# Optimization experiments

Measured on AMD Instinct MI355X. Metric: run time of the kernel, lower is better.

The kernel has to match this reference:

```python
import jax, jax.numpy as jnp
import numpy as np

FEATS = 768
HEAD = 12
HD = FEATS // HEAD


def setup_inputs() -> dict:
    key = jax.random.key(0)
    ks = jax.random.split(key, 10)
    b, n, f = 8, 1024, FEATS
    s = 1.0 / np.sqrt(f)
    return {
        "x": jax.random.normal(ks[0], (b, n, f), dtype=jnp.float32),
        "bias": jnp.zeros((), dtype=jnp.float32),
        "Wq": jax.random.normal(ks[1], (f, f), dtype=jnp.float32) * s,
        "bq": jnp.zeros((f,), dtype=jnp.float32),
        "Wk": jax.random.normal(ks[2], (f, f), dtype=jnp.float32) * s,
        "bk": jnp.zeros((f,), dtype=jnp.float32),
        "Wv": jax.random.normal(ks[3], (f, f), dtype=jnp.float32) * s,
        "bv": jnp.zeros((f,), dtype=jnp.float32),
        "Wo": jax.random.normal(ks[4], (f, f), dtype=jnp.float32) * s,
        "bo": jnp.zeros((f,), dtype=jnp.float32),
    }


def reference(x, bias, Wq, bq, Wk, bk, Wv, bv, Wo, bo):
    b, n, f = x.shape
    sqrt_d = jnp.sqrt(jnp.asarray(f, dtype=x.dtype))  # scale uses full feats, per source

    def split_heads(t):  # (b,n,f) -> (b,h,n,hd)
        return t.reshape(b, n, HEAD, HD).transpose(0, 2, 1, 3)

    q = split_heads(x @ Wq.T + bq)
    k = split_heads(x @ Wk.T + bk)
    v = split_heads(x @ Wv.T + bv)

    # sigmoid attention: no row-wise normalization
    score = jax.nn.sigmoid(jnp.einsum('bhif,bhjf->bhij', q, k) / sqrt_d + bias)
    attn = jnp.einsum('bhij,bhjf->bihf', score, v)  # (b,n,h,hd)
    o = attn.reshape(b, n, f) @ Wo.T + bo  # dropout p=0.0 -> identity
    return o
```

## Files before the change

### kernel.cpp

```cpp
#include <hip/hip_runtime.h>

#define FEATS 768
#define NHEAD 12
#define HD    64
#define SEQ   1024
#define NB    8
#define MROWS (NB*SEQ)
#define NQK   (2*FEATS)
#define QKVN  (3*FEATS)
#define QSC   0.0520616136f

typedef __attribute__((ext_vector_type(8))) __bf16          bf16x8;
typedef __attribute__((ext_vector_type(4))) __bf16          bf16x4;
typedef __attribute__((ext_vector_type(4))) unsigned short  us4;
typedef __attribute__((ext_vector_type(4))) float           f32x4;

__device__ __forceinline__ unsigned short f2bf(float f) {
  union { float f; unsigned u; } v; v.f = f;
  return (unsigned short)((v.u + 0x7fffu + ((v.u >> 16) & 1u)) >> 16);
}

__device__ __forceinline__ void gload_lds16(const void* g, void* l) {
  __builtin_amdgcn_global_load_lds(
      (const __attribute__((address_space(1))) void*)g,
      (__attribute__((address_space(3))) void*)l, 16, 0, 0);
}

__global__ void cast_all(const float* __restrict__ x,
                         const float* __restrict__ Wq, const float* __restrict__ Wk,
                         const float* __restrict__ Wv, const float* __restrict__ Wo,
                         const float* __restrict__ bq, const float* __restrict__ bk,
                         const float* __restrict__ bv,
                         unsigned short* __restrict__ Xbf,
                         unsigned short* __restrict__ Wcat,
                         unsigned short* __restrict__ Wobf,
                         float* __restrict__ bcat) {
  int blk = blockIdx.x;
  if (blk < 6144) {
    int i = blk * 256 + threadIdx.x;
    f32x4 v = ((const f32x4*)x)[i];
    us4 o;
    o[0] = f2bf(v[0]); o[1] = f2bf(v[1]); o[2] = f2bf(v[2]); o[3] = f2bf(v[3]);
    ((us4*)Xbf)[i] = o;
  } else if (blk < 8448) {
    int bb = blk - 6144;
    int mtx = bb / 576;
    int i = (bb % 576) * 256 + threadIdx.x;
    const float* src = (mtx == 0) ? Wq : (mtx == 1) ? Wk : (mtx == 2) ? Wv : Wo;
    f32x4 v = ((const f32x4*)src)[i];
    us4 o;
    o[0] = f2bf(v[0]); o[1] = f2bf(v[1]); o[2] = f2bf(v[2]); o[3] = f2bf(v[3]);
    if (mtx < 3) ((us4*)Wcat)[mtx * 147456 + i] = o;
    else         ((us4*)Wobf)[i] = o;
  } else {
    int i = (blk - 8448) * 256 + threadIdx.x;
    if (i < QKVN)
      bcat[i] = (i < FEATS) ? bq[i] : (i < 2*FEATS ? bk[i-FEATS] : bv[i-2*FEATS]);
  }
}

#define FOFF(row) ((row)*64 + (((g) ^ (((row) >> 1) & 3)) << 4))

__global__ __launch_bounds__(256, 3) void gemm1_bt(
    const unsigned short* __restrict__ A,
    const unsigned short* __restrict__ B,
    const float* __restrict__ bias,
    unsigned short* __restrict__ QKo,
    unsigned short* __restrict__ VTo)
{
  __shared__ __align__(16) char Al[2 * 8192];
  __shared__ __align__(16) char Bl[2 * 12288];

  const int tid  = threadIdx.x;
  const int lane = tid & 63;
  const int w    = tid >> 6;
  const int l15  = lane & 15;
  const int g    = lane >> 4;
  const int wm   = (w >> 1) * 64;
  const int wn   = (w & 1) * 96;

  const int id  = blockIdx.x;
  const int xcd = id & 7;
  const int j   = id >> 3;
  const int mi  = xcd * 8 + (j & 7);
  const int ni  = j >> 3;
  const int mbase = mi * 128;
  const int nbase = ni * 192;

  const int trow  = tid >> 2;
  const int sslot = ((tid & 3) ^ ((tid >> 3) & 3)) * 8;
  const unsigned short* Ag = A + (size_t)(mbase + trow) * 768 + sslot;
  const unsigned short* Bg = B + (size_t)(nbase + trow) * 768 + sslot;

  auto STAGE = [&](int buf, int t) {
    const unsigned short* sa = Ag + t * 32;
    const unsigned short* sb = Bg + t * 32;
    char* da = Al + buf * 8192  + tid * 16;
    char* db = Bl + buf * 12288 + tid * 16;
    gload_lds16(sa,            da);
    gload_lds16(sa + 64*768,   da + 4096);
    gload_lds16(sb,            db);
    gload_lds16(sb + 64*768,   db + 4096);
    gload_lds16(sb + 128*768,  db + 8192);
  };

  f32x4 acc[4][6] = {};

  STAGE(0, 0);
  asm volatile("s_waitcnt vmcnt(0)" ::: "memory");
  __builtin_amdgcn_s_barrier();

  for (int t = 0; t < 24; t++) {
    if (t < 23) STAGE((t + 1) & 1, t + 1);

    const char* Ab = Al + (t & 1) * 8192;
    const char* Bb = Bl + (t & 1) * 12288;
    bf16x8 af[4];
#pragma unroll
    for (int mf = 0; mf < 4; mf++) {
      const int row = wm + mf*16 + l15;
      af[mf] = *(const bf16x8*)(Ab + FOFF(row));
    }
    __builtin_amdgcn_s_setprio(1);
#pragma unroll
    for (int nf = 0; nf < 6; nf++) {
      const int row = wn + nf*16 + l15;
      bf16x8 bfv = *(const bf16x8*)(Bb + FOFF(row));
#pragma unroll
      for (int mf = 0; mf < 4; mf++)
        acc[mf][nf] = __builtin_amdgcn_mfma_f32_16x16x32_bf16(af[mf], bfv, acc[mf][nf], 0, 0, 0);
    }
    __builtin_amdgcn_s_setprio(0);

    if (t < 23) {
      asm volatile("s_waitcnt vmcnt(0)" ::: "memory");
      __builtin_amdgcn_s_barrier();
    }
  }

  const bool isQK = (ni < 8);
  const float osc = (ni < 4) ? QSC : 1.0f;
#pragma unroll
  for (int mf = 0; mf < 4; mf++)
#pragma unroll
    for (int nf = 0; nf < 6; nf++) {
      const int col  = nbase + wn + nf*16 + l15;
      const float bb = bias[col];
      const int row0 = mbase + wm + mf*16 + g*4;
      if (isQK) {
#pragma unroll
        for (int r = 0; r < 4; r++)
          QKo[(size_t)(row0 + r)*NQK + col] = f2bf((acc[mf][nf][r] + bb) * osc);
      } else {
        const int c  = col - NQK;
        const int hh = c >> 6, dd = c & 63;
        const int bI = row0 >> 10, n0 = row0 & 1023;
        us4 o;
#pragma unroll
        for (int r = 0; r < 4; r++) o[r] = f2bf(acc[mf][nf][r] + bb);
        *(us4*)(VTo + ((size_t)((bI*NHEAD + hh)*HD + dd))*SEQ + n0) = o;
      }
    }
}

__global__ __launch_bounds__(256, 4) void gemm2_bt(
    const unsigned short* __restrict__ A,
    const unsigned short* __restrict__ B,
    const float* __restrict__ bias,
    float* __restrict__ C)
{
  __shared__ __align__(16) char Al[2 * 4096];
  __shared__ __align__(16) char Bl[2 * 8192];

  const int tid  = threadIdx.x;
  const int lane = tid & 63;
  const int w    = tid >> 6;
  const int l15  = lane & 15;
  const int g    = lane >> 4;
  const int wm   = (w >> 1) * 32;
  const int wn   = (w & 1) * 64;

  const int id  = blockIdx.x;
  const int xcd = id & 7;
  const int j   = id >> 3;
  const int mi  = xcd * 16 + (j & 15);
  const int ni  = j >> 4;
  const int mbase = mi * 64;
  const int nbase = ni * 128;

  const int trow  = tid >> 2;
  const int sslot = ((tid & 3) ^ ((tid >> 3) & 3)) * 8;
  const unsigned short* Ag = A + (size_t)(mbase + trow) * 768 + sslot;
  const unsigned short* Bg = B + (size_t)(nbase + trow) * 768 + sslot;

  auto STAGE = [&](int buf, int t) {
    const unsigned short* sa = Ag + t * 32;
    const unsigned short* sb = Bg + t * 32;
    char* da = Al + buf * 4096 + tid * 16;
    char* db = Bl + buf * 8192 + tid * 16;
    gload_lds16(sa,           da);
    gload_lds16(sb,           db);
    gload_lds16(sb + 64*768,  db + 4096);
  };

  f32x4 acc[2][4] = {};

  STAGE(0, 0);
  asm volatile("s_waitcnt vmcnt(0)" ::: "memory");
  __builtin_amdgcn_s_barrier();

  for (int t = 0; t < 24; t++) {
    if (t < 23) STAGE((t + 1) & 1, t + 1);

    const char* Ab = Al + (t & 1) * 4096;
    const char* Bb = Bl + (t & 1) * 8192;
    bf16x8 af[2], bfv[4];
#pragma unroll
    for (int mf = 0; mf < 2; mf++) {
      const int row = wm + mf*16 + l15;
      af[mf] = *(const bf16x8*)(Ab + FOFF(row));
    }
#pragma unroll
    for (int nf = 0; nf < 4; nf++) {
      const int row = wn + nf*16 + l15;
      bfv[nf] = *(const bf16x8*)(Bb + FOFF(row));
    }
    __builtin_amdgcn_s_setprio(1);
#pragma unroll
    for (int mf = 0; mf < 2; mf++)
#pragma unroll
      for (int nf = 0; nf < 4; nf++)
        acc[mf][nf] = __builtin_amdgcn_mfma_f32_16x16x32_bf16(af[mf], bfv[nf], acc[mf][nf], 0, 0, 0);
    __builtin_amdgcn_s_setprio(0);

    if (t < 23) {
      asm volatile("s_waitcnt vmcnt(0)" ::: "memory");
      __builtin_amdgcn_s_barrier();
    }
  }

#pragma unroll
  for (int mf = 0; mf < 2; mf++)
#pragma unroll
    for (int nf = 0; nf < 4; nf++) {
      const int col  = nbase + wn + nf*16 + l15;
      const float bb = bias[col];
      const int row0 = mbase + wm + mf*16 + g*4;
#pragma unroll
      for (int r = 0; r < 4; r++)
        C[(size_t)(row0 + r)*FEATS + col] = acc[mf][nf][r] + bb;
    }
}
#undef FOFF

__global__ __launch_bounds__(256, 3) void attn_kernel(
    const unsigned short* __restrict__ QK,
    const unsigned short* __restrict__ VT,
    const float* __restrict__ biasp,
    unsigned short* __restrict__ AO)
{
  __shared__ __align__(16) char Kl[2][8192];
  __shared__ __align__(16) char Vl[2][8192];
  __shared__ __align__(16) char Sl[4][4096];

  const int tid  = threadIdx.x;
  const int lane = tid & 63;
  const int w    = tid >> 6;
  const int l15  = lane & 15;
  const int g    = lane >> 4;

  const int id  = blockIdx.x;
  const int r8  = id & 7;
  const int m   = id >> 3;
  const int bh  = r8 * 12 + (m >> 3);
  const int qx  = m & 7;
  const int b   = bh / NHEAD;
  const int h   = bh % NHEAD;
  const int rowB  = b * SEQ;
  const int qbase = rowB + qx * 128;

  const float Kb = __builtin_amdgcn_exp2f(-biasp[0] * 1.4426950408889634f);

  bf16x8 qf[2][2];
  {
    const unsigned short* qp = QK + (size_t)(qbase + w*32 + l15) * NQK + h*HD + g*8;
    qf[0][0] = *(const bf16x8*)(qp);
    qf[0][1] = *(const bf16x8*)(qp + 32);
    qf[1][0] = *(const bf16x8*)(qp + 16*NQK);
    qf[1][1] = *(const bf16x8*)(qp + 16*NQK + 32);
  }

  const int trow = tid >> 3;
  const int colb = ((tid & 7) * 16) ^ ((trow & 7) << 4);
  const char* Ksrc = (const char*)QK +
      ((size_t)(rowB + trow) * NQK + FEATS + h*HD) * 2 + colb;
  const char* Vsrc = (const char*)VT +
      ((size_t)(bh*HD + trow)) * (SEQ*2) + colb;

  auto STAGE = [&](int p, int t) {
    char* kw = Kl[p] + tid*16;
    char* vw = Vl[p] + tid*16;
    gload_lds16(Ksrc + (size_t)t * 64 * (NQK*2),                kw);
    gload_lds16(Ksrc + (size_t)t * 64 * (NQK*2) + 32*(NQK*2),   kw + 4096);
    gload_lds16(Vsrc + t * 128,                                 vw);
    gload_lds16(Vsrc + t * 128 + 32*(SEQ*2),                    vw + 4096);
  };

  char* Sw = Sl[w];
  f32x4 o_acc[4][2] = {};

  STAGE(0, 0);
  __syncthreads();

  for (int t = 0; t < 16; t++) {
    const int p = t & 1;
    if (t < 15) STAGE(p ^ 1, t + 1);

    const char* Kp = Kl[p];
    f32x4 sT[2][4] = {};
    __builtin_amdgcn_s_setprio(1);
#pragma unroll
    for (int nf = 0; nf < 4; nf++)
#pragma unroll
      for (int ks = 0; ks < 2; ks++) {
        const int row = nf*16 + l15;
        const int by  = (row*128 + ks*64 + g*16) ^ ((row & 7) << 4);
        bf16x8 kf = *(const bf16x8*)(Kp + by);
        sT[0][nf] = __builtin_amdgcn_mfma_f32_16x16x32_bf16(kf, qf[0][ks], sT[0][nf], 0, 0, 0);
        sT[1][nf] = __builtin_amdgcn_mfma_f32_16x16x32_bf16(kf, qf[1][ks], sT[1][nf], 0, 0, 0);
      }
    __builtin_amdgcn_s_setprio(0);

    const char* Vp = Vl[p];
    bf16x8 vf[4][2];
#pragma unroll
    for (int df = 0; df < 4; df++)
#pragma unroll
      for (int js = 0; js < 2; js++) {
        const int row = df*16 + l15;
        const int by  = (row*128 + js*64 + g*16) ^ ((row & 7) << 4);
        vf[df][js] = *(const bf16x8*)(Vp + by);
      }

#pragma unroll
    for (int qm = 0; qm < 2; qm++)
#pragma unroll
      for (int nf = 0; nf < 4; nf++) {
        bf16x4 pk;
#pragma unroll
        for (int rr = 0; rr < 4; rr++) {
          const float e = __builtin_amdgcn_exp2f(-sT[qm][nf][rr]);
          pk[rr] = (__bf16)__builtin_amdgcn_rcpf(__builtin_fmaf(Kb, e, 1.0f));
        }
        const int sq = qm*16 + l15;
        const int by = (sq*128 + (nf*16 + g*4)*2) ^ ((sq & 7) << 4);
        *(bf16x4*)(Sw + by) = pk;
      }

    __builtin_amdgcn_s_setprio(1);
#pragma unroll
    for (int js = 0; js < 2; js++) {
      bf16x8 sf[2];
#pragma unroll
      for (int qm = 0; qm < 2; qm++) {
        const int sq = qm*16 + l15;
        const int by = (sq*128 + js*64 + g*16) ^ ((sq & 7) << 4);
        sf[qm] = *(const bf16x8*)(Sw + by);
      }
#pragma unroll
      for (int df = 0; df < 4; df++)
#pragma unroll
        for (int qm = 0; qm < 2; qm++)
          o_acc[df][qm] = __builtin_amdgcn_mfma_f32_16x16x32_bf16(vf[df][js], sf[qm], o_acc[df][qm], 0, 0, 0);
    }
    __builtin_amdgcn_s_setprio(0);

    __syncthreads();
  }

  unsigned short* aop = AO + (size_t)(qbase + w*32) * FEATS + h*HD;
#pragma unroll
  for (int df = 0; df < 4; df++)
#pragma unroll
    for (int qm = 0; qm < 2; qm++) {
      const int q  = qm*16 + l15;
      const int d0 = df*16 + g*4;
      bf16x4 o;
#pragma unroll
      for (int rr = 0; rr < 4; rr++) o[rr] = (__bf16)o_acc[df][qm][rr];
      *(bf16x4*)(aop + (size_t)q * FEATS + d0) = o;
    }
}

extern "C" void kernel_launch(void* const* d_in, const int* in_sizes, int n_in,
                              void* d_out, int out_size, void* d_ws, size_t ws_size,
                              hipStream_t stream) {
  const float* x    = (const float*)d_in[0];
  const float* bias = (const float*)d_in[1];
  const float* Wq   = (const float*)d_in[2];
  const float* bq   = (const float*)d_in[3];
  const float* Wk   = (const float*)d_in[4];
  const float* bk   = (const float*)d_in[5];
  const float* Wv   = (const float*)d_in[6];
  const float* bv   = (const float*)d_in[7];
  const float* Wo   = (const float*)d_in[8];
  const float* bo   = (const float*)d_in[9];
  float* out = (float*)d_out;

  char* ws = (char*)d_ws;
  unsigned short* Xbf  = (unsigned short*)(ws + 0);
  unsigned short* Wcat = (unsigned short*)(ws + 12582912);
  unsigned short* Wobf = (unsigned short*)(ws + 16121856);
  float*          bcat = (float*)        (ws + 17301504);
  unsigned short* QKb  = (unsigned short*)(ws + 17310720);
  unsigned short* VTb  = (unsigned short*)(ws + 42476544);
  unsigned short* AO   = Xbf;

  cast_all<<<8457, 256, 0, stream>>>(x, Wq, Wk, Wv, Wo, bq, bk, bv,
                                     Xbf, Wcat, Wobf, bcat);

  gemm1_bt<<<768, 256, 0, stream>>>(Xbf, Wcat, bcat, QKb, VTb);

  attn_kernel<<<768, 256, 0, stream>>>(QKb, VTb, bias, AO);

  gemm2_bt<<<768, 256, 0, stream>>>(AO, Wobf, bo, out);
}
```

Baseline: 108.6 us.

## Software-pipeline attention loop: overlap QK^T of tile t with sigmoid·V of t-1

Restructures the sigmoid-attention inner loop so each iteration computes the QK^T MFMAs for tile t while applying sigmoid and the PV MFMAs for tile t-1. Score accumulators ping-pong between two register sets, and K and V staging are split so V is loaded one tile later than K. The goal is to hide exp/rcp and LDS latency behind MFMA work and to keep the matrix units busy. In exchange it needs more accumulator registers, which can lower occupancy, and the schedule is more complex.

```diff
diff --git a/kernel.cpp b/kernel.cpp
--- a/kernel.cpp
+++ b/kernel.cpp
@@ -297,51 +297,22 @@
   const char* Vsrc = (const char*)VT +
       ((size_t)(bh*HD + trow)) * (SEQ*2) + colb;
 
-  auto STAGE = [&](int p, int t) {
+  auto STAGE_K = [&](int p, int t) {
     char* kw = Kl[p] + tid*16;
+    gload_lds16(Ksrc + (size_t)t * 64 * (NQK*2),              kw);
+    gload_lds16(Ksrc + (size_t)t * 64 * (NQK*2) + 32*(NQK*2), kw + 4096);
+  };
+  auto STAGE_V = [&](int p, int t) {
     char* vw = Vl[p] + tid*16;
-    gload_lds16(Ksrc + (size_t)t * 64 * (NQK*2),                kw);
-    gload_lds16(Ksrc + (size_t)t * 64 * (NQK*2) + 32*(NQK*2),   kw + 4096);
-    gload_lds16(Vsrc + t * 128,                                 vw);
-    gload_lds16(Vsrc + t * 128 + 32*(SEQ*2),                    vw + 4096);
+    gload_lds16(Vsrc + t * 128,              vw);
+    gload_lds16(Vsrc + t * 128 + 32*(SEQ*2), vw + 4096);
   };
 
   char* Sw = Sl[w];
   f32x4 o_acc[4][2] = {};
-
-  STAGE(0, 0);
-  __syncthreads();
-
-  for (int t = 0; t < 16; t++) {
-    const int p = t & 1;
-    if (t < 15) STAGE(p ^ 1, t + 1);
-
-    const char* Kp = Kl[p];
-    f32x4 sT[2][4] = {};
-    __builtin_amdgcn_s_setprio(1);
-#pragma unroll
-    for (int nf = 0; nf < 4; nf++)
-#pragma unroll
-      for (int ks = 0; ks < 2; ks++) {
-        const int row = nf*16 + l15;
-        const int by  = (row*128 + ks*64 + g*16) ^ ((row & 7) << 4);
-        bf16x8 kf = *(const bf16x8*)(Kp + by);
-        sT[0][nf] = __builtin_amdgcn_mfma_f32_16x16x32_bf16(kf, qf[0][ks], sT[0][nf], 0, 0, 0);
-        sT[1][nf] = __builtin_amdgcn_mfma_f32_16x16x32_bf16(kf, qf[1][ks], sT[1][nf], 0, 0, 0);
-      }
-    __builtin_amdgcn_s_setprio(0);
-
-    const char* Vp = Vl[p];
-    bf16x8 vf[4][2];
-#pragma unroll
-    for (int df = 0; df < 4; df++)
-#pragma unroll
-      for (int js = 0; js < 2; js++) {
-        const int row = df*16 + l15;
-        const int by  = (row*128 + js*64 + g*16) ^ ((row & 7) << 4);
-        vf[df][js] = *(const bf16x8*)(Vp + by);
-      }
-
+  f32x4 sE[2][4], sO[2][4];
+
+  auto SIGPV = [&](f32x4 (&sP)[2][4], const char* Vp) {
 #pragma unroll
     for (int qm = 0; qm < 2; qm++)
 #pragma unroll
@@ -349,15 +320,13 @@
         bf16x4 pk;
 #pragma unroll
         for (int rr = 0; rr < 4; rr++) {
-          const float e = __builtin_amdgcn_exp2f(-sT[qm][nf][rr]);
+          const float e = __builtin_amdgcn_exp2f(-sP[qm][nf][rr]);
           pk[rr] = (__bf16)__builtin_amdgcn_rcpf(__builtin_fmaf(Kb, e, 1.0f));
         }
         const int sq = qm*16 + l15;
         const int by = (sq*128 + (nf*16 + g*4)*2) ^ ((sq & 7) << 4);
         *(bf16x4*)(Sw + by) = pk;
       }
-
-    __builtin_amdgcn_s_setprio(1);
 #pragma unroll
     for (int js = 0; js < 2; js++) {
       bf16x8 sf[2];
@@ -367,16 +336,62 @@
         const int by = (sq*128 + js*64 + g*16) ^ ((sq & 7) << 4);
         sf[qm] = *(const bf16x8*)(Sw + by);
       }
+      bf16x8 vf[4];
+#pragma unroll
+      for (int df = 0; df < 4; df++) {
+        const int row = df*16 + l15;
+        const int by  = (row*128 + js*64 + g*16) ^ ((row & 7) << 4);
+        vf[df] = *(const bf16x8*)(Vp + by);
+      }
+      __builtin_amdgcn_s_setprio(1);
 #pragma unroll
       for (int df = 0; df < 4; df++)
 #pragma unroll
         for (int qm = 0; qm < 2; qm++)
-          o_acc[df][qm] = __builtin_amdgcn_mfma_f32_16x16x32_bf16(vf[df][js], sf[qm], o_acc[df][qm], 0, 0, 0);
-    }
+          o_acc[df][qm] = __builtin_amdgcn_mfma_f32_16x16x32_bf16(vf[df], sf[qm], o_acc[df][qm], 0, 0, 0);
+      __builtin_amdgcn_s_setprio(0);
+    }
+  };
+
+  auto BODY = [&](int t, f32x4 (&sC)[2][4], f32x4 (&sP)[2][4], bool stK, bool doPrev) {
+    if (stK) STAGE_K((t + 1) & 1, t + 1);
+    STAGE_V(t & 1, t);
+
+    const char* Kp = Kl[t & 1];
+#pragma unroll
+    for (int qm = 0; qm < 2; qm++)
+#pragma unroll
+      for (int nf = 0; nf < 4; nf++)
+        sC[qm][nf] = (f32x4){0.f, 0.f, 0.f, 0.f};
+    __builtin_amdgcn_s_setprio(1);
+#pragma unroll
+    for (int nf = 0; nf < 4; nf++)
+#pragma unroll
+      for (int ks = 0; ks < 2; ks++) {
+        const int row = nf*16 + l15;
+        const int by  = (row*128 + ks*64 + g*16) ^ ((row & 7) << 4);
+        bf16x8 kf = *(const bf16x8*)(Kp + by);
+        sC[0][nf] = __builtin_amdgcn_mfma_f32_16x16x32_bf16(kf, qf[0][ks], sC[0][nf], 0, 0, 0);
+        sC[1][nf] = __builtin_amdgcn_mfma_f32_16x16x32_bf16(kf, qf[1][ks], sC[1][nf], 0, 0, 0);
+      }
     __builtin_amdgcn_s_setprio(0);
 
+    if (doPrev) SIGPV(sP, Vl[(t - 1) & 1]);
+
     __syncthreads();
+  };
+
+  STAGE_K(0, 0);
+  __syncthreads();
+
+  BODY(0, sE, sO, true, false);
+#pragma unroll 1
+  for (int t = 1; t < 15; t += 2) {
+    BODY(t,     sO, sE, true, true);
+    BODY(t + 1, sE, sO, true, true);
   }
+  BODY(15, sO, sE, false, true);
+  SIGPV(sO, Vl[1]);
 
   unsigned short* aop = AO + (size_t)(qbase + w*32) * FEATS + h*HD;
 #pragma unroll
```

Result: no change. 108.1 us (-0.5%).
